# Optimization experiments

Hardware: AMD Instinct MI355X
Metric: run time of the kernel (lower is better)

## Reference

```python
import jax, jax.numpy as jnp
import numpy as np

B, S, D = 2, 2048, 2048
H, KV = 16, 4
HD = D // H          # 128
G = H // KV          # 4
EPS = 1e-5


def _rms_norm(t, w):
    # standard RMSNorm over last dim (intended math of the module's qk norm)
    return t * jax.lax.rsqrt(jnp.mean(t * t, axis=-1, keepdims=True) + EPS) * w


def _rope(t, cos, sin):
    # t: [b, h, s, hd]; cos/sin: [s, hd]
    hd = t.shape[-1]
    t1, t2 = t[..., : hd // 2], t[..., hd // 2 :]
    rot = jnp.concatenate([-t2, t1], axis=-1)
    return t * cos[None, None] + rot * sin[None, None]


def setup_inputs() -> dict:
    key = jax.random.key(0)
    ks = jax.random.split(key, 8)
    x = jax.random.normal(ks[0], (B, S, D), dtype=jnp.float32)
    # causal mask: True = masked out
    mask = jnp.triu(jnp.ones((S, S), dtype=bool), k=1)
    # RoPE tables
    inv_freq = 1.0 / (10000.0 ** (np.arange(0, HD, 2, dtype=np.float32) / HD))
    ang = np.arange(S, dtype=np.float32)[:, None] * inv_freq[None, :]  # [S, HD/2]
    ang = np.concatenate([ang, ang], axis=-1)                          # [S, HD]
    cos = jnp.asarray(np.cos(ang))
    sin = jnp.asarray(np.sin(ang))
    sc = 1.0 / np.sqrt(D)
    W_q = jax.random.normal(ks[1], (D, D), dtype=jnp.float32) * sc
    W_k = jax.random.normal(ks[2], (KV * HD, D), dtype=jnp.float32) * sc
    W_v = jax.random.normal(ks[3], (KV * HD, D), dtype=jnp.float32) * sc
    W_o = jax.random.normal(ks[4], (D, D), dtype=jnp.float32) * sc
    q_norm_w = jnp.ones((HD,), dtype=jnp.float32)
    k_norm_w = jnp.ones((HD,), dtype=jnp.float32)
    return {"x": x, "mask": mask, "cos": cos, "sin": sin,
            "W_q": W_q, "W_k": W_k, "W_v": W_v, "W_o": W_o,
            "q_norm_w": q_norm_w, "k_norm_w": k_norm_w}


def reference(x, mask, cos, sin, W_q, W_k, W_v, W_o, q_norm_w, k_norm_w):
    b, s, d = x.shape
    q = (x @ W_q.T).reshape(b, s, H, HD).transpose(0, 2, 1, 3)   # [b,H,s,hd]
    k = (x @ W_k.T).reshape(b, s, KV, HD).transpose(0, 2, 1, 3)  # [b,KV,s,hd]
    v = (x @ W_v.T).reshape(b, s, KV, HD).transpose(0, 2, 1, 3)
    q = _rms_norm(q, q_norm_w)
    k = _rms_norm(k, k_norm_w)
    q = _rope(q, cos, sin)
    k = _rope(k, cos, sin)
    # GQA: group queries by kv head, avoid materializing expanded K/V
    qg = q.reshape(b, KV, G, s, HD)
    scores = jnp.einsum("bkgqd,bktd->bkgqt", qg, k) / jnp.sqrt(jnp.float32(HD))
    scores = jnp.where(mask[None, None, None], -jnp.inf, scores)
    att = jax.nn.softmax(scores, axis=-1)
    ctx = jnp.einsum("bkgqt,bktd->bkgqd", att, v)
    ctx = ctx.reshape(b, H, s, HD).transpose(0, 2, 1, 3).reshape(b, s, d)
    return ctx @ W_o.T
```

## Files before the change

### kernel.cpp

```cpp
#include <hip/hip_runtime.h>

typedef unsigned short u16;
typedef __bf16 bf16x8 __attribute__((ext_vector_type(8)));
typedef float f32x4 __attribute__((ext_vector_type(4)));
typedef u16 u16x8 __attribute__((ext_vector_type(8)));
typedef u16 u16x4 __attribute__((ext_vector_type(4)));

static constexpr int S_LEN  = 2048;
static constexpr int DMODEL = 2048;
static constexpr int NKV    = 4;
static constexpr int HD     = 128;

__device__ __forceinline__ u16 f2bf(float f) {
  unsigned u = __builtin_bit_cast(unsigned, f);
  u += 0x7fffu + ((u >> 16) & 1u);
  return (u16)(u >> 16);
}
__device__ __forceinline__ float bf2f(u16 h) {
  unsigned u = ((unsigned)h) << 16;
  return __builtin_bit_cast(float, u);
}
__device__ __forceinline__ bf16x8 as_bf(u16x8 v) { return __builtin_bit_cast(bf16x8, v); }

__device__ __forceinline__ u16x8 cvt8(const float* p) {
  f32x4 lo = *(const f32x4*)p;
  f32x4 hi = *(const f32x4*)(p + 4);
  u16x8 r;
#pragma unroll
  for (int j = 0; j < 4; ++j) { r[j] = f2bf(lo[j]); r[j + 4] = f2bf(hi[j]); }
  return r;
}

__device__ __forceinline__ void gld16(const u16* g, u16* l) {
  auto gp = (const __attribute__((address_space(1))) unsigned*)(unsigned long long)g;
  auto lp = (__attribute__((address_space(3))) unsigned*)(unsigned)(unsigned long long)l;
  __builtin_amdgcn_global_load_lds(gp, lp, 16, 0, 0);
}

__global__ __launch_bounds__(256) void cvt1(const float* __restrict__ in,
                                            u16* __restrict__ out, int n8) {
  const int i = blockIdx.x * 256 + threadIdx.x;
  if (i < n8) *(u16x8*)(out + (long)i * 8) = cvt8(in + (long)i * 8);
}
__global__ __launch_bounds__(256) void cvt3(const float* __restrict__ a,
                                            const float* __restrict__ b,
                                            const float* __restrict__ c,
                                            u16* __restrict__ out) {
  const int i = blockIdx.x * 256 + threadIdx.x;
  const float* src; long j;
  if (i < 524288)      { src = a; j = i; }
  else if (i < 655360) { src = b; j = i - 524288; }
  else                 { src = c; j = i - 655360; }
  *(u16x8*)(out + (long)i * 8) = cvt8(src + j * 8);
}

__global__ __launch_bounds__(256) void gemm_qkv(
    const u16* __restrict__ A, const u16* __restrict__ Bw,
    u16* __restrict__ Cq, u16* __restrict__ Ck, u16* __restrict__ Cv)
{
  constexpr int K = 2048;
  __shared__ u16 As[128 * 32];
  __shared__ u16 Bs[128 * 32];
  const int bx = blockIdx.x;
  const int bm = bx / 24, bn = bx % 24;
  const int tid = threadIdx.x, wave = tid >> 6, lane = tid & 63;
  const int wm = (wave & 1) << 6, wn = (wave >> 1) << 6;
  const long m0 = (long)bm << 7, n0 = (long)bn << 7;

  f32x4 acc[4][4] = {};

  const int srow = (wave << 5) + (lane >> 2);
  const int sch  = (lane & 3) << 3;
  const u16* ga = A  + (m0 + srow) * K + sch;
  const u16* gb = Bw + (n0 + srow) * K + sch;
  u16* la = As + (wave << 10);
  u16* lb = Bs + (wave << 10);
  const long rstep = (long)16 * K;

  const int fr = lane & 15, fc = (lane >> 4) << 3;

  for (int k0 = 0; k0 < K; k0 += 32) {
    __syncthreads();
    gld16(ga + k0,         la);
    gld16(ga + k0 + rstep, la + 512);
    gld16(gb + k0,         lb);
    gld16(gb + k0 + rstep, lb + 512);
    __syncthreads();
    bf16x8 af[4], bf[4];
#pragma unroll
    for (int i = 0; i < 4; ++i)
      af[i] = as_bf(*(const u16x8*)&As[(wm + (i << 4) + fr) * 32 + fc]);
#pragma unroll
    for (int i = 0; i < 4; ++i)
      bf[i] = as_bf(*(const u16x8*)&Bs[(wn + (i << 4) + fr) * 32 + fc]);
#pragma unroll
    for (int mi = 0; mi < 4; ++mi)
#pragma unroll
      for (int ni = 0; ni < 4; ++ni)
        acc[mi][ni] = __builtin_amdgcn_mfma_f32_16x16x32_bf16(af[mi], bf[ni], acc[mi][ni], 0, 0, 0);
  }

  u16* Cb; int N2; long c0;
  if (bn < 16)      { Cb = Cq; N2 = 2048; c0 = n0; }
  else if (bn < 20) { Cb = Ck; N2 = 512;  c0 = n0 - 2048; }
  else              { Cb = Cv; N2 = 512;  c0 = n0 - 2560; }

  const int er = (lane >> 4) << 2, ec = lane & 15;
#pragma unroll
  for (int mi = 0; mi < 4; ++mi)
#pragma unroll
    for (int ni = 0; ni < 4; ++ni) {
      u16* cp = Cb + (m0 + wm + (mi << 4) + er) * N2 + (c0 + wn + (ni << 4) + ec);
#pragma unroll
      for (int r = 0; r < 4; ++r)
        cp[(long)r * N2] = f2bf(acc[mi][ni][r]);
    }
}

__global__ __launch_bounds__(256) void gemm_o(
    const u16* __restrict__ A, const u16* __restrict__ Bw, float* __restrict__ C)
{
  constexpr int K = 2048, N = 2048;
  __shared__ u16 As[128 * 32];
  __shared__ u16 Bs[128 * 32];
  const int bx = blockIdx.x;
  const int bm = bx >> 4, bn = bx & 15;
  const int tid = threadIdx.x, wave = tid >> 6, lane = tid & 63;
  const int wm = (wave & 1) << 6, wn = (wave >> 1) << 6;
  const long m0 = (long)bm << 7, n0 = (long)bn << 7;

  f32x4 acc[4][4] = {};

  const int srow = (wave << 5) + (lane >> 2);
  const int sch  = (lane & 3) << 3;
  const u16* ga = A  + (m0 + srow) * K + sch;
  const u16* gb = Bw + (n0 + srow) * K + sch;
  u16* la = As + (wave << 10);
  u16* lb = Bs + (wave << 10);
  const long rstep = (long)16 * K;

  const int fr = lane & 15, fc = (lane >> 4) << 3;

  for (int k0 = 0; k0 < K; k0 += 32) {
    __syncthreads();
    gld16(ga + k0,         la);
    gld16(ga + k0 + rstep, la + 512);
    gld16(gb + k0,         lb);
    gld16(gb + k0 + rstep, lb + 512);
    __syncthreads();
    bf16x8 af[4], bf[4];
#pragma unroll
    for (int i = 0; i < 4; ++i)
      af[i] = as_bf(*(const u16x8*)&As[(wm + (i << 4) + fr) * 32 + fc]);
#pragma unroll
    for (int i = 0; i < 4; ++i)
      bf[i] = as_bf(*(const u16x8*)&Bs[(wn + (i << 4) + fr) * 32 + fc]);
#pragma unroll
    for (int mi = 0; mi < 4; ++mi)
#pragma unroll
      for (int ni = 0; ni < 4; ++ni)
        acc[mi][ni] = __builtin_amdgcn_mfma_f32_16x16x32_bf16(af[mi], bf[ni], acc[mi][ni], 0, 0, 0);
  }

  const int er = (lane >> 4) << 2, ec = lane & 15;
#pragma unroll
  for (int mi = 0; mi < 4; ++mi)
#pragma unroll
    for (int ni = 0; ni < 4; ++ni) {
      float* cp = C + (m0 + wm + (mi << 4) + er) * N + (n0 + wn + (ni << 4) + ec);
#pragma unroll
      for (int r = 0; r < 4; ++r)
        cp[(long)r * N] = acc[mi][ni][r];
    }
}

__global__ __launch_bounds__(256) void norm_rope(
    u16* __restrict__ buf, const float* __restrict__ w,
    const float* __restrict__ cosb, const float* __restrict__ sinb,
    int sshift, float scale)
{
  const int row  = blockIdx.x * 4 + (threadIdx.x >> 6);
  const int lane = threadIdx.x & 63;
  const int s = (row >> sshift) & (S_LEN - 1);
  u16* p = buf + (long)row * HD;
  float t1 = bf2f(p[lane]), t2 = bf2f(p[lane + 64]);
  float ss = t1 * t1 + t2 * t2;
#pragma unroll
  for (int off = 32; off; off >>= 1) ss += __shfl_xor(ss, off);
  const float r = rsqrtf(ss * (1.0f / 128.0f) + 1e-5f);
  t1 *= r * w[lane];
  t2 *= r * w[lane + 64];
  const float* cp = cosb + s * HD;
  const float* sp = sinb + s * HD;
  const float o1 = (t1 * cp[lane]      - t2 * sp[lane])      * scale;
  const float o2 = (t2 * cp[lane + 64] + t1 * sp[lane + 64]) * scale;
  p[lane]      = f2bf(o1);
  p[lane + 64] = f2bf(o2);
}

__global__ __launch_bounds__(256) void transpose_v(const u16* __restrict__ v,
                                                   u16* __restrict__ vt)
{
  const int idx = blockIdx.x * 256 + threadIdx.x;
  const int t   = idx & (S_LEN - 1);
  const int hd0 = ((idx >> 11) & 15) << 3;
  const int bkv = idx >> 15;
  const u16* vp = v + ((long)(bkv >> 2) * S_LEN + t) * 512 + ((bkv & 3) << 7) + hd0;
  u16x8 d = *(const u16x8*)vp;
  u16* op = vt + ((long)bkv * HD + hd0) * S_LEN + t;
#pragma unroll
  for (int j = 0; j < 8; ++j) op[(long)j * S_LEN] = d[j];
}

__global__ __launch_bounds__(256, 2) void flash(
    const u16* __restrict__ q, const u16* __restrict__ k,
    const u16* __restrict__ vt, u16* __restrict__ ctx)
{
  __shared__ u16 Ks[128 * 128];
  __shared__ u16 Vs[128 * 128];
  const int tid = threadIdx.x, wave = tid >> 6, lane = tid & 63;
  const int bx  = blockIdx.x;
  const int qtr = bx & 15;
  const int bh  = bx >> 4;
  const int qt  = (bx < 256) ? (15 - qtr) : qtr;
  const int b   = bh >> 4, h = bh & 15;
  const int kv  = h >> 2;
  const int q0  = qt << 7;

  const int fr = lane & 15, fhi = lane >> 4;

  bf16x8 qf[2][4];
#pragma unroll
  for (int nq = 0; nq < 2; ++nq) {
    const long s = q0 + (wave << 5) + (nq << 4) + fr;
    const u16* qp = q + ((long)b * S_LEN + s) * DMODEL + h * HD;
#pragma unroll
    for (int kb = 0; kb < 4; ++kb)
      qf[nq][kb] = as_bf(*(const u16x8*)(qp + (kb << 5) + (fhi << 3)));
  }

  f32x4 O[8][2] = {};
  float mS[2] = {-1e30f, -1e30f}, lS[2] = {0.f, 0.f};

  const u16* kbase = k + ((long)b * S_LEN) * 512 + kv * HD;
  const u16* vbase = vt + ((long)(b * NKV + kv)) * HD * S_LEN;

  for (int jt = 0; jt <= qt; ++jt) {
    const int t0 = jt << 7;
    __syncthreads();
#pragma unroll
    for (int i = 0; i < 8; ++i) {
      const int row = (wave << 5) + (i << 2) + fhi;
      const int gc  = fr ^ (row & 15);
      gld16(kbase + (long)(t0 + row) * 512 + (gc << 3),
            Ks + (((wave << 5) + (i << 2)) << 7));
      gld16(vbase + (long)row * S_LEN + t0 + (gc << 3),
            Vs + (((wave << 5) + (i << 2)) << 7));
    }
    __syncthreads();

    f32x4 Sac[8][2] = {};
#pragma unroll
    for (int mt = 0; mt < 8; ++mt) {
      const int t = (mt << 4) + fr;
      bf16x8 kf[4];
#pragma unroll
      for (int kb = 0; kb < 4; ++kb) {
        const int cc = ((kb << 2) + fhi) ^ (t & 15);
        kf[kb] = as_bf(*(const u16x8*)&Ks[t * 128 + (cc << 3)]);
      }
#pragma unroll
      for (int nq = 0; nq < 2; ++nq)
#pragma unroll
        for (int kb = 0; kb < 4; ++kb)
          Sac[mt][nq] = __builtin_amdgcn_mfma_f32_16x16x32_bf16(kf[kb], qf[nq][kb], Sac[mt][nq], 0, 0, 0);
    }

    if (jt == qt) {
      const int tb = fhi << 2;
#pragma unroll
      for (int mt = 0; mt < 8; ++mt)
#pragma unroll
        for (int nq = 0; nq < 2; ++nq) {
          const int qin = (wave << 5) + (nq << 4) + fr;
#pragma unroll
          for (int r = 0; r < 4; ++r)
            if ((mt << 4) + tb + r > qin) Sac[mt][nq][r] = -1e30f;
        }
    }

#pragma unroll
    for (int nq = 0; nq < 2; ++nq) {
      float rmax = -1e30f;
#pragma unroll
      for (int mt = 0; mt < 8; ++mt)
#pragma unroll
        for (int r = 0; r < 4; ++r) rmax = fmaxf(rmax, Sac[mt][nq][r]);
      rmax = fmaxf(rmax, __shfl_xor(rmax, 16));
      rmax = fmaxf(rmax, __shfl_xor(rmax, 32));
      const float mn = fmaxf(mS[nq], rmax);
      const float al = __expf(mS[nq] - mn);
      mS[nq] = mn;
      float rsum = 0.f;
#pragma unroll
      for (int mt = 0; mt < 8; ++mt)
#pragma unroll
        for (int r = 0; r < 4; ++r) {
          const float e = __expf(Sac[mt][nq][r] - mn);
          Sac[mt][nq][r] = e;
          rsum += e;
        }
      rsum += __shfl_xor(rsum, 16);
      rsum += __shfl_xor(rsum, 32);
      lS[nq] = lS[nq] * al + rsum;
#pragma unroll
      for (int mh = 0; mh < 8; ++mh)
#pragma unroll
        for (int r = 0; r < 4; ++r) O[mh][nq][r] *= al;
    }

    __syncthreads();

#pragma unroll
    for (int nq = 0; nq < 2; ++nq) {
      const int qrow = (wave << 5) + (nq << 4) + fr;
#pragma unroll
      for (int mt = 0; mt < 8; ++mt) {
        u16x4 pk;
#pragma unroll
        for (int r = 0; r < 4; ++r) pk[r] = f2bf(Sac[mt][nq][r]);
        const int c8 = (mt << 1) + (fhi >> 1);
        const int cs = c8 ^ (fr & 7);
        *(u16x4*)&Ks[qrow * 128 + (cs << 3) + ((fhi & 1) << 2)] = pk;
      }
    }
    asm volatile("" ::: "memory");

    bf16x8 pf[2][4];
#pragma unroll
    for (int nq = 0; nq < 2; ++nq) {
      const int qrow = (wave << 5) + (nq << 4) + fr;
#pragma unroll
      for (int kt = 0; kt < 4; ++kt) {
        const int cs = ((kt << 2) + fhi) ^ (fr & 7);
        pf[nq][kt] = as_bf(*(const u16x8*)&Ks[qrow * 128 + (cs << 3)]);
      }
    }
#pragma unroll
    for (int mh = 0; mh < 8; ++mh) {
      const int hd = (mh << 4) + fr;
      bf16x8 vf[4];
#pragma unroll
      for (int kt = 0; kt < 4; ++kt) {
        const int cc = ((kt << 2) + fhi) ^ (hd & 15);
        vf[kt] = as_bf(*(const u16x8*)&Vs[hd * 128 + (cc << 3)]);
      }
#pragma unroll
      for (int nq = 0; nq < 2; ++nq)
#pragma unroll
        for (int kt = 0; kt < 4; ++kt)
          O[mh][nq] = __builtin_amdgcn_mfma_f32_16x16x32_bf16(vf[kt], pf[nq][kt], O[mh][nq], 0, 0, 0);
    }
  }

#pragma unroll
  for (int nq = 0; nq < 2; ++nq) {
    const float inv = 1.0f / lS[nq];
    const long s = q0 + (wave << 5) + (nq << 4) + fr;
    u16* cp = ctx + ((long)b * S_LEN + s) * DMODEL + h * HD;
#pragma unroll
    for (int mh = 0; mh < 8; ++mh) {
      u16x4 pk;
#pragma unroll
      for (int r = 0; r < 4; ++r) pk[r] = f2bf(O[mh][nq][r] * inv);
      *(u16x4*)(cp + (mh << 4) + (fhi << 2)) = pk;
    }
  }
}

extern "C" void kernel_launch(void* const* d_in, const int* in_sizes, int n_in,
                              void* d_out, int out_size, void* d_ws, size_t ws_size,
                              hipStream_t stream) {
  const float* x    = (const float*)d_in[0];
  const float* cosb = (const float*)d_in[2];
  const float* sinb = (const float*)d_in[3];
  const float* Wq   = (const float*)d_in[4];
  const float* Wk   = (const float*)d_in[5];
  const float* Wv   = (const float*)d_in[6];
  const float* Wo   = (const float*)d_in[7];
  const float* qw   = (const float*)d_in[8];
  const float* kw   = (const float*)d_in[9];

  u16* qb  = (u16*)d_out;
  u16* xb  = qb + 8388608;
  u16* kb  = (u16*)d_ws;
  u16* vb  = kb  + 2097152;
  u16* vtb = vb  + 2097152;
  u16* ctx = vtb + 2097152;
  u16* wall = ctx;
  u16* wob  = kb;
  float* out = (float*)d_out;

  cvt1<<<dim3(4096), dim3(256), 0, stream>>>(x, xb, 1048576);
  cvt3<<<dim3(3072), dim3(256), 0, stream>>>(Wq, Wk, Wv, wall);
  gemm_qkv<<<dim3(768), dim3(256), 0, stream>>>(xb, wall, qb, kb, vb);
  norm_rope<<<dim3(16384), dim3(256), 0, stream>>>(qb, qw, cosb, sinb, 4, 0.08838834764831845f);
  norm_rope<<<dim3(4096),  dim3(256), 0, stream>>>(kb, kw, cosb, sinb, 2, 1.0f);
  transpose_v<<<dim3(1024), dim3(256), 0, stream>>>(vb, vtb);
  flash<<<dim3(512), dim3(256), 0, stream>>>(qb, kb, vtb, ctx);
  cvt1<<<dim3(2048), dim3(256), 0, stream>>>(Wo, wob, 524288);
  gemm_o<<<dim3(512), dim3(256), 0, stream>>>(ctx, wob, out);
}
```

Baseline: 348.2 us.

## Split flash attention KV range across two blocks and merge partials

Each query tile is now handled by two blocks, each taking alternating 64-wide KV tiles. Each block writes its unnormalized context plus row max and row sum, and a new merge kernel combines the two halves. This doubles the grid and halves the shared memory per block, allowing three blocks per CU, to improve occupancy and load balance on the causal workload. The cost is an extra kernel pass over the context, plus rounding the partial outputs to bf16 before the merge. The V transpose kernel is also rewritten so each thread handles an 8x8 block with vectorized stores instead of scattered 2-byte writes.

```diff
diff --git a/kernel.cpp b/kernel.cpp
--- a/kernel.cpp
+++ b/kernel.cpp
@@ -202,30 +202,40 @@
                                                    u16* __restrict__ vt)
 {
   const int idx = blockIdx.x * 256 + threadIdx.x;
-  const int t   = idx & (S_LEN - 1);
-  const int hd0 = ((idx >> 11) & 15) << 3;
-  const int bkv = idx >> 15;
-  const u16* vp = v + ((long)(bkv >> 2) * S_LEN + t) * 512 + ((bkv & 3) << 7) + hd0;
-  u16x8 d = *(const u16x8*)vp;
-  u16* op = vt + ((long)bkv * HD + hd0) * S_LEN + t;
-#pragma unroll
-  for (int j = 0; j < 8; ++j) op[(long)j * S_LEN] = d[j];
-}
-
-__global__ __launch_bounds__(256, 2) void flash(
+  const int t0  = (idx & 255) << 3;
+  const int hd0 = ((idx >> 8) & 15) << 3;
+  const int bkv = idx >> 12;
+  const u16* vp = v + ((long)(bkv >> 2) * S_LEN + t0) * 512 + ((bkv & 3) << 7) + hd0;
+  u16x8 rw[8];
+#pragma unroll
+  for (int c = 0; c < 8; ++c) rw[c] = *(const u16x8*)(vp + (long)c * 512);
+  u16* op = vt + ((long)bkv * HD + hd0) * S_LEN + t0;
+#pragma unroll
+  for (int j = 0; j < 8; ++j) {
+    u16x8 o;
+#pragma unroll
+    for (int c = 0; c < 8; ++c) o[c] = rw[c][j];
+    *(u16x8*)(op + (long)j * S_LEN) = o;
+  }
+}
+
+__global__ __launch_bounds__(256, 3) void flash(
     const u16* __restrict__ q, const u16* __restrict__ k,
-    const u16* __restrict__ vt, u16* __restrict__ ctx)
-{
-  __shared__ u16 Ks[128 * 128];
-  __shared__ u16 Vs[128 * 128];
+    const u16* __restrict__ vt, u16* __restrict__ ctx0,
+    u16* __restrict__ ctx1, float* __restrict__ ml)
+{
+  __shared__ u16 Ks[64 * 128];
+  __shared__ u16 Vs[128 * 64];
   const int tid = threadIdx.x, wave = tid >> 6, lane = tid & 63;
   const int bx  = blockIdx.x;
-  const int qtr = bx & 15;
-  const int bh  = bx >> 4;
-  const int qt  = (bx < 256) ? (15 - qtr) : qtr;
+  const int par = bx & 1;
+  const int qtr = (bx >> 1) & 15;
+  const int bh  = bx >> 5;
+  const int qt  = (bh < 16) ? (15 - qtr) : qtr;
   const int b   = bh >> 4, h = bh & 15;
   const int kv  = h >> 2;
   const int q0  = qt << 7;
+  u16* ctx = par ? ctx1 : ctx0;
 
   const int fr = lane & 15, fhi = lane >> 4;
 
@@ -245,23 +255,28 @@
   const u16* kbase = k + ((long)b * S_LEN) * 512 + kv * HD;
   const u16* vbase = vt + ((long)(b * NKV + kv)) * HD * S_LEN;
 
-  for (int jt = 0; jt <= qt; ++jt) {
-    const int t0 = jt << 7;
-    __syncthreads();
-#pragma unroll
-    for (int i = 0; i < 8; ++i) {
-      const int row = (wave << 5) + (i << 2) + fhi;
+  for (int jt = par; jt <= 2 * qt + 1; jt += 2) {
+    const int t0 = jt << 6;
+    __syncthreads();
+#pragma unroll
+    for (int i = 0; i < 4; ++i) {
+      const int row = (wave << 4) + (i << 2) + fhi;
       const int gc  = fr ^ (row & 15);
       gld16(kbase + (long)(t0 + row) * 512 + (gc << 3),
-            Ks + (((wave << 5) + (i << 2)) << 7));
-      gld16(vbase + (long)row * S_LEN + t0 + (gc << 3),
-            Vs + (((wave << 5) + (i << 2)) << 7));
-    }
-    __syncthreads();
-
-    f32x4 Sac[8][2] = {};
-#pragma unroll
-    for (int mt = 0; mt < 8; ++mt) {
+            Ks + (((wave << 4) + (i << 2)) << 7));
+    }
+#pragma unroll
+    for (int i = 0; i < 4; ++i) {
+      const int row = (wave << 5) + (i << 3) + (lane >> 3);
+      const int gc8 = (lane & 7) ^ (row & 7);
+      gld16(vbase + (long)row * S_LEN + t0 + (gc8 << 3),
+            Vs + (((wave << 5) + (i << 3)) << 6));
+    }
+    __syncthreads();
+
+    f32x4 Sac[4][2] = {};
+#pragma unroll
+    for (int mt = 0; mt < 4; ++mt) {
       const int t = (mt << 4) + fr;
       bf16x8 kf[4];
 #pragma unroll
@@ -276,16 +291,16 @@
           Sac[mt][nq] = __builtin_amdgcn_mfma_f32_16x16x32_bf16(kf[kb], qf[nq][kb], Sac[mt][nq], 0, 0, 0);
     }
 
-    if (jt == qt) {
-      const int tb = fhi << 2;
-#pragma unroll
-      for (int mt = 0; mt < 8; ++mt)
+    if ((jt >> 1) == qt) {
+      const int tbase = ((jt & 1) << 6) + (fhi << 2);
+#pragma unroll
+      for (int mt = 0; mt < 4; ++mt)
 #pragma unroll
         for (int nq = 0; nq < 2; ++nq) {
           const int qin = (wave << 5) + (nq << 4) + fr;
 #pragma unroll
           for (int r = 0; r < 4; ++r)
-            if ((mt << 4) + tb + r > qin) Sac[mt][nq][r] = -1e30f;
+            if ((mt << 4) + tbase + r > qin) Sac[mt][nq][r] = -1e30f;
         }
     }
 
@@ -293,7 +308,7 @@
     for (int nq = 0; nq < 2; ++nq) {
       float rmax = -1e30f;
 #pragma unroll
-      for (int mt = 0; mt < 8; ++mt)
+      for (int mt = 0; mt < 4; ++mt)
 #pragma unroll
         for (int r = 0; r < 4; ++r) rmax = fmaxf(rmax, Sac[mt][nq][r]);
       rmax = fmaxf(rmax, __shfl_xor(rmax, 16));
@@ -303,7 +318,7 @@
       mS[nq] = mn;
       float rsum = 0.f;
 #pragma unroll
-      for (int mt = 0; mt < 8; ++mt)
+      for (int mt = 0; mt < 4; ++mt)
 #pragma unroll
         for (int r = 0; r < 4; ++r) {
           const float e = __expf(Sac[mt][nq][r] - mn);
@@ -325,57 +340,83 @@
     for (int nq = 0; nq < 2; ++nq) {
       const int qrow = (wave << 5) + (nq << 4) + fr;
 #pragma unroll
-      for (int mt = 0; mt < 8; ++mt) {
+      for (int mt = 0; mt < 4; ++mt) {
         u16x4 pk;
 #pragma unroll
         for (int r = 0; r < 4; ++r) pk[r] = f2bf(Sac[mt][nq][r]);
-        const int c8 = (mt << 1) + (fhi >> 1);
-        const int cs = c8 ^ (fr & 7);
-        *(u16x4*)&Ks[qrow * 128 + (cs << 3) + ((fhi & 1) << 2)] = pk;
+        const int cs = ((mt << 1) + (fhi >> 1)) ^ (fr & 7);
+        *(u16x4*)&Ks[qrow * 64 + (cs << 3) + ((fhi & 1) << 2)] = pk;
       }
     }
     asm volatile("" ::: "memory");
 
-    bf16x8 pf[2][4];
+    bf16x8 pf[2][2];
 #pragma unroll
     for (int nq = 0; nq < 2; ++nq) {
       const int qrow = (wave << 5) + (nq << 4) + fr;
 #pragma unroll
-      for (int kt = 0; kt < 4; ++kt) {
+      for (int kt = 0; kt < 2; ++kt) {
         const int cs = ((kt << 2) + fhi) ^ (fr & 7);
-        pf[nq][kt] = as_bf(*(const u16x8*)&Ks[qrow * 128 + (cs << 3)]);
+        pf[nq][kt] = as_bf(*(const u16x8*)&Ks[qrow * 64 + (cs << 3)]);
       }
     }
 #pragma unroll
     for (int mh = 0; mh < 8; ++mh) {
       const int hd = (mh << 4) + fr;
-      bf16x8 vf[4];
-#pragma unroll
-      for (int kt = 0; kt < 4; ++kt) {
-        const int cc = ((kt << 2) + fhi) ^ (hd & 15);
-        vf[kt] = as_bf(*(const u16x8*)&Vs[hd * 128 + (cc << 3)]);
+      bf16x8 vf[2];
+#pragma unroll
+      for (int kt = 0; kt < 2; ++kt) {
+        const int cc = ((kt << 2) + fhi) ^ (hd & 7);
+        vf[kt] = as_bf(*(const u16x8*)&Vs[hd * 64 + (cc << 3)]);
       }
 #pragma unroll
       for (int nq = 0; nq < 2; ++nq)
 #pragma unroll
-        for (int kt = 0; kt < 4; ++kt)
+        for (int kt = 0; kt < 2; ++kt)
           O[mh][nq] = __builtin_amdgcn_mfma_f32_16x16x32_bf16(vf[kt], pf[nq][kt], O[mh][nq], 0, 0, 0);
     }
   }
 
 #pragma unroll
   for (int nq = 0; nq < 2; ++nq) {
-    const float inv = 1.0f / lS[nq];
-    const long s = q0 + (wave << 5) + (nq << 4) + fr;
-    u16* cp = ctx + ((long)b * S_LEN + s) * DMODEL + h * HD;
+    const int qabs = q0 + (wave << 5) + (nq << 4) + fr;
+    u16* cp = ctx + ((long)b * S_LEN + qabs) * DMODEL + h * HD;
 #pragma unroll
     for (int mh = 0; mh < 8; ++mh) {
       u16x4 pk;
 #pragma unroll
-      for (int r = 0; r < 4; ++r) pk[r] = f2bf(O[mh][nq][r] * inv);
+      for (int r = 0; r < 4; ++r) pk[r] = f2bf(O[mh][nq][r]);
       *(u16x4*)(cp + (mh << 4) + (fhi << 2)) = pk;
     }
-  }
+    if (fhi == 0) {
+      float* mlp = ml + ((((long)bh << 11) + qabs) << 2) + (par << 1);
+      mlp[0] = mS[nq];
+      mlp[1] = lS[nq];
+    }
+  }
+}
+
+__global__ __launch_bounds__(256) void merge(
+    const u16* __restrict__ c0, const u16* __restrict__ c1,
+    const float* __restrict__ ml, u16* __restrict__ out)
+{
+  const int idx = blockIdx.x * 256 + threadIdx.x;
+  const long e8 = (long)idx << 3;
+  const int bq = (int)(e8 >> 11);
+  const int h  = ((int)e8 & 2047) >> 7;
+  const int b  = bq >> 11, s = bq & 2047;
+  const float* mlp = ml + ((((long)(b * 16 + h) << 11) + s) << 2);
+  const float m0 = mlp[0], l0 = mlp[1], m1 = mlp[2], l1 = mlp[3];
+  const float m  = fmaxf(m0, m1);
+  const float a0 = __expf(m0 - m), a1 = __expf(m1 - m);
+  const float inv = 1.0f / (l0 * a0 + l1 * a1);
+  u16x8 x0 = *(const u16x8*)(c0 + e8);
+  u16x8 x1 = *(const u16x8*)(c1 + e8);
+  u16x8 o;
+#pragma unroll
+  for (int j = 0; j < 8; ++j)
+    o[j] = f2bf((bf2f(x0[j]) * a0 + bf2f(x1[j]) * a1) * inv);
+  *(u16x8*)(out + e8) = o;
 }
 
 extern "C" void kernel_launch(void* const* d_in, const int* in_sizes, int n_in,
@@ -391,14 +432,16 @@
   const float* qw   = (const float*)d_in[8];
   const float* kw   = (const float*)d_in[9];
 
-  u16* qb  = (u16*)d_out;
-  u16* xb  = qb + 8388608;
-  u16* kb  = (u16*)d_ws;
-  u16* vb  = kb  + 2097152;
-  u16* vtb = vb  + 2097152;
-  u16* ctx = vtb + 2097152;
-  u16* wall = ctx;
+  u16* qb   = (u16*)d_out;
+  u16* xb   = qb + 8388608;
+  u16* ctx1 = xb;
+  u16* kb   = (u16*)d_ws;
+  u16* vb   = kb  + 2097152;
+  u16* vtb  = vb  + 2097152;
+  u16* ctx0 = vtb + 2097152;
+  u16* wall = ctx0;
   u16* wob  = kb;
+  float* ml = (float*)(ctx0 + 8388608);
   float* out = (float*)d_out;
 
   cvt1<<<dim3(4096), dim3(256), 0, stream>>>(x, xb, 1048576);
@@ -406,8 +449,9 @@
   gemm_qkv<<<dim3(768), dim3(256), 0, stream>>>(xb, wall, qb, kb, vb);
   norm_rope<<<dim3(16384), dim3(256), 0, stream>>>(qb, qw, cosb, sinb, 4, 0.08838834764831845f);
   norm_rope<<<dim3(4096),  dim3(256), 0, stream>>>(kb, kw, cosb, sinb, 2, 1.0f);
-  transpose_v<<<dim3(1024), dim3(256), 0, stream>>>(vb, vtb);
-  flash<<<dim3(512), dim3(256), 0, stream>>>(qb, kb, vtb, ctx);
+  transpose_v<<<dim3(128), dim3(256), 0, stream>>>(vb, vtb);
+  flash<<<dim3(1024), dim3(256), 0, stream>>>(qb, kb, vtb, ctx0, ctx1, ml);
+  merge<<<dim3(4096), dim3(256), 0, stream>>>(ctx0, ctx1, ml, ctx0);
   cvt1<<<dim3(2048), dim3(256), 0, stream>>>(Wo, wob, 524288);
-  gemm_o<<<dim3(512), dim3(256), 0, stream>>>(ctx, wob, out);
-}
+  gemm_o<<<dim3(512), dim3(256), 0, stream>>>(ctx0, wob, out);
+}
```

Result: slower. 410.4 us (+17.9%).
